# Kernel optimization log

Measured on AMD Instinct MI355X. Metric: run time of the kernel, lower is better.

## Reference

```python
import jax, jax.numpy as jnp
import numpy as np

B, T, C, H = 4, 2048, 1024, 16


def setup_inputs() -> dict:
    key = jax.random.key(0)
    ks = jax.random.split(key, 8)
    s = 0.02
    return {
        "xq": jax.random.normal(ks[0], (B, T, C), jnp.float32),
        "xk": jax.random.normal(ks[1], (B, T, C), jnp.float32),
        "xv": jax.random.normal(ks[2], (B, T, C), jnp.float32),
        "Wq": jax.random.normal(ks[3], (C, C), jnp.float32) * s,
        "Wk": jax.random.normal(ks[4], (C, C), jnp.float32) * s,
        "Wv": jax.random.normal(ks[5], (C, C), jnp.float32) * s,
        "Wo": jax.random.normal(ks[6], (C, C), jnp.float32) * s,
        "bo": jnp.zeros((C,), jnp.float32),
    }


def reference(xq, xk, xv, Wq, Wk, Wv, Wo, bo):
    # torch nn.Linear: y = x @ W.T
    q = xq @ Wq.T  # (B,T,C)
    k = xk @ Wk.T
    v = xv @ Wv.T
    hd = C // H
    # (B,T,C) -> (B,H,T,hd)
    q = q.reshape(B, T, H, hd).transpose(0, 2, 1, 3)
    k = k.reshape(B, T, H, hd).transpose(0, 2, 1, 3)
    v = v.reshape(B, T, H, hd).transpose(0, 2, 1, 3)
    scale = 1.0 / jnp.sqrt(jnp.asarray(hd, q.dtype))
    att = jnp.einsum("bhqd,bhkd->bhqk", q, k) * scale  # (B,H,T,T)
    causal = jnp.tril(jnp.ones((T, T), bool))
    att = jnp.where(causal, att, jnp.asarray(-jnp.inf, att.dtype))
    att = jax.nn.softmax(att, axis=-1)
    y = jnp.einsum("bhqk,bhkd->bhqd", att, v)  # (B,H,T,hd)
    y = y.transpose(0, 2, 1, 3).reshape(B, T, C)
    return y @ Wo.T + bo
```

## Files before the change

### kernel.cpp

```cpp
#include <hip/hip_runtime.h>
#include <stdint.h>

#define B_ 4
#define T_ 2048
#define C_ 1024
#define H_ 16
#define HD 64

typedef __attribute__((ext_vector_type(8))) short bf16x8;
typedef __attribute__((ext_vector_type(4))) short bf16x4;
typedef __attribute__((ext_vector_type(4))) float v4f;
typedef __attribute__((ext_vector_type(4))) uint32_t v4u;

static __device__ __forceinline__ short f2bf(float f) {
    union { float f; uint32_t u; } v; v.f = f;
    uint32_t u = v.u;
    uint32_t r = (u + 0x7fffu + ((u >> 16) & 1u)) >> 16;
    return (short)(r & 0xffffu);
}
static __device__ __forceinline__ uint32_t pack2(float x, float y) {
    uint32_t a = __float_as_uint(x) + 0x8000u;
    uint32_t b = __float_as_uint(y) + 0x8000u;
    return __builtin_amdgcn_perm(b, a, 0x07060302u);
}
static __device__ __forceinline__ uint32_t pack2t(float x, float y) {
    return __builtin_amdgcn_perm(__float_as_uint(y), __float_as_uint(x), 0x07060302u);
}
static __device__ __forceinline__ void gload_lds16(const void* g, void* l) {
    __builtin_amdgcn_global_load_lds(
        (const __attribute__((address_space(1))) void*)g,
        (__attribute__((address_space(3))) void*)l, 16, 0, 0);
}

__global__ __launch_bounds__(256) void convx(
    const float* __restrict__ x0, const float* __restrict__ x1,
    short* __restrict__ o0, short* __restrict__ o1,
    const float* __restrict__ w0, const float* __restrict__ w1,
    const float* __restrict__ w2, const float* __restrict__ w3,
    short* __restrict__ wout)
{
    int bid = blockIdx.x;
    const float* src; short* dst; size_t id;
    if (bid < 8192) {
        src = (bid < 4096) ? x0 : x1;
        dst = (bid < 4096) ? o0 : o1;
        id = (size_t)(bid & 4095) * 256 + threadIdx.x;
    } else {
        int wb = bid - 8192;
        int wi = wb >> 9;
        src = (wi == 0) ? w0 : (wi == 1) ? w1 : (wi == 2) ? w2 : w3;
        dst = wout + (size_t)wi * (C_ * C_);
        id = (size_t)(wb & 511) * 256 + threadIdx.x;
    }
    const float* p = src + id * 8;
    v4f a0 = *(const v4f*)p, a1 = *(const v4f*)(p + 4);
    v4u dv;
    dv[0] = pack2(a0[0], a0[1]); dv[1] = pack2(a0[2], a0[3]);
    dv[2] = pack2(a1[0], a1[1]); dv[3] = pack2(a1[2], a1[3]);
    *(v4u*)&dst[id * 8] = dv;
}


__global__ __launch_bounds__(256) void proj_gemm(
    const short* __restrict__ Xq, const short* __restrict__ Xk,
    const short* __restrict__ Wb, const float* __restrict__ xv,
    short* __restrict__ Qh, short* __restrict__ Kh, short* __restrict__ Vt,
    float qscale)
{
    const int K = 1024;
    __shared__ short As[128 * 64];
    __shared__ short Bs[128 * 64];
    const int t = threadIdx.x;
    const int w = t >> 6, l = t & 63, g = l >> 4, c = l & 15;
    const int wm = w & 1, wn = w >> 1;
    const int z = blockIdx.z;
    const int m0 = (z == 2 ? blockIdx.y : blockIdx.x) * 128;
    const int n0 = (z == 2 ? blockIdx.x : blockIdx.y) * 128;
    const short* Ab = (z == 0) ? Xq : (z == 1) ? Xk : (Wb + 2 * C_ * C_);
    const short* Bb = (z == 0) ? Wb : (Wb + C_ * C_);

    const int srow = l >> 3;
    const int sch = (l & 7) ^ (l >> 3);
    const int rch = c & 7;

    v4f acc[4][4];
#pragma unroll
    for (int i = 0; i < 4; ++i)
#pragma unroll
        for (int j = 0; j < 4; ++j) acc[i][j] = (v4f){0.f, 0.f, 0.f, 0.f};

    for (int k0 = 0; k0 < K; k0 += 64) {
        __syncthreads();
#pragma unroll
        for (int i = 0; i < 4; ++i) {
            int sp = w * 4 + i;
            gload_lds16(Ab + (size_t)(m0 + sp * 8 + srow) * K + k0 + sch * 8,
                        &As[sp * 512]);
        }
        if (z < 2) {
#pragma unroll
            for (int i = 0; i < 4; ++i) {
                int sp = w * 4 + i;
                gload_lds16(Bb + (size_t)(n0 + sp * 8 + srow) * K + k0 + sch * 8,
                            &Bs[sp * 512]);
            }
        } else {
#pragma unroll
            for (int i = 0; i < 4; ++i) {
                int id = i * 256 + t;
                int rr = id >> 3, cc = id & 7;
                const float* p = xv + (size_t)(n0 + rr) * K + k0 + cc * 8;
                v4f a0 = *(const v4f*)p, a1 = *(const v4f*)(p + 4);
                v4u dv;
                dv[0] = pack2(a0[0], a0[1]); dv[1] = pack2(a0[2], a0[3]);
                dv[2] = pack2(a1[0], a1[1]); dv[3] = pack2(a1[2], a1[3]);
                *(v4u*)&Bs[rr * 64 + ((cc ^ (rr & 7)) * 8)] = dv;
            }
        }
        __syncthreads();
#pragma unroll
        for (int s = 0; s < 2; ++s) {
            const int kch = ((4 * s + g) ^ rch) * 8;
            bf16x8 af[4], bfr[4];
#pragma unroll
            for (int i = 0; i < 4; ++i)
                af[i] = *(const bf16x8*)&As[(wm * 64 + i * 16 + c) * 64 + kch];
#pragma unroll
            for (int j = 0; j < 4; ++j)
                bfr[j] = *(const bf16x8*)&Bs[(wn * 64 + j * 16 + c) * 64 + kch];
#pragma unroll
            for (int i = 0; i < 4; ++i)
#pragma unroll
                for (int j = 0; j < 4; ++j)
                    acc[i][j] = __builtin_amdgcn_mfma_f32_16x16x32_bf16(af[i], bfr[j], acc[i][j], 0, 0, 0);
        }
    }
    if (z < 2) {
        short* Out = (z == 0) ? Qh : Kh;
        const float os = (z == 0) ? qscale : 1.0f;
#pragma unroll
        for (int i = 0; i < 4; ++i)
#pragma unroll
            for (int j = 0; j < 4; ++j)
#pragma unroll
                for (int r = 0; r < 4; ++r) {
                    int m = m0 + wm * 64 + i * 16 + g * 4 + r;
                    int n = n0 + wn * 64 + j * 16 + c;
                    int b = m >> 11, tt = m & (T_ - 1);
                    int h = n >> 6, d = n & 63;
                    Out[((size_t)(b * H_ + h) * T_ + tt) * HD + d] = f2bf(acc[i][j][r] * os);
                }
    } else {
#pragma unroll
        for (int i = 0; i < 4; ++i)
#pragma unroll
            for (int j = 0; j < 4; ++j)
#pragma unroll
                for (int r = 0; r < 4; ++r) {
                    int m = m0 + wm * 64 + i * 16 + g * 4 + r;
                    int n = n0 + wn * 64 + j * 16 + c;
                    int b = n >> 11, tt = n & (T_ - 1);
                    int h = m >> 6, d = m & 63;
                    Vt[((size_t)(b * H_ + h) * HD + d) * T_ + tt] = f2bf(acc[i][j][r]);
                }
    }
}

__global__ __launch_bounds__(256) void gemm_o(
    const short* __restrict__ Yb, const short* __restrict__ Wo,
    float* __restrict__ Out, const float* __restrict__ bias)
{
    const int K = 1024;
    __shared__ short As[128 * 64];
    __shared__ short Bs[128 * 64];
    const int t = threadIdx.x;
    const int w = t >> 6, l = t & 63, g = l >> 4, c = l & 15;
    const int wm = w & 1, wn = w >> 1;
    const int m0 = blockIdx.x * 128, n0 = blockIdx.y * 128;

    const int srow = l >> 3;
    const int sch = (l & 7) ^ (l >> 3);
    const int rch = c & 7;

    v4f acc[4][4];
#pragma unroll
    for (int i = 0; i < 4; ++i)
#pragma unroll
        for (int j = 0; j < 4; ++j) acc[i][j] = (v4f){0.f, 0.f, 0.f, 0.f};

    for (int k0 = 0; k0 < K; k0 += 64) {
        __syncthreads();
#pragma unroll
        for (int i = 0; i < 4; ++i) {
            int sp = w * 4 + i;
            gload_lds16(Yb + (size_t)(m0 + sp * 8 + srow) * K + k0 + sch * 8,
                        &As[sp * 512]);
            gload_lds16(Wo + (size_t)(n0 + sp * 8 + srow) * K + k0 + sch * 8,
                        &Bs[sp * 512]);
        }
        __syncthreads();
#pragma unroll
        for (int s = 0; s < 2; ++s) {
            const int kch = ((4 * s + g) ^ rch) * 8;
            bf16x8 af[4], bfr[4];
#pragma unroll
            for (int i = 0; i < 4; ++i)
                af[i] = *(const bf16x8*)&As[(wm * 64 + i * 16 + c) * 64 + kch];
#pragma unroll
            for (int j = 0; j < 4; ++j)
                bfr[j] = *(const bf16x8*)&Bs[(wn * 64 + j * 16 + c) * 64 + kch];
#pragma unroll
            for (int i = 0; i < 4; ++i)
#pragma unroll
                for (int j = 0; j < 4; ++j)
                    acc[i][j] = __builtin_amdgcn_mfma_f32_16x16x32_bf16(af[i], bfr[j], acc[i][j], 0, 0, 0);
        }
    }
#pragma unroll
    for (int i = 0; i < 4; ++i)
#pragma unroll
        for (int j = 0; j < 4; ++j)
#pragma unroll
            for (int r = 0; r < 4; ++r) {
                int m = m0 + wm * 64 + i * 16 + g * 4 + r;
                int n = n0 + wn * 64 + j * 16 + c;
                Out[(size_t)m * C_ + n] = acc[i][j][r] + bias[n];
            }
}

__global__ __launch_bounds__(256) void attn_kernel(
    const short* __restrict__ Q, const short* __restrict__ Kp,
    const short* __restrict__ Vt, short* __restrict__ Y)
{
    __shared__ short Ks[2 * 64 * 32];
    __shared__ short Vs[64 * 72];
    const int t = threadIdx.x;
    const int w = t >> 6, l = t & 63, g = l >> 4, c = l & 15;
    const int bid = blockIdx.x;
    const int slot = bid >> 3;
    const int p = slot & 15;
    const size_t bh = (size_t)((bid & 7) * 8 + (slot >> 4));

    const int srow = l >> 2;
    const int sch = (l & 3) ^ ((l >> 3) & 3);
    const int gs = (g ^ ((c >> 1) & 3)) * 8;

    bf16x8 ones;
#pragma unroll
    for (int i = 0; i < 8; ++i) ones[i] = (short)0x3F80;

    const int qtL = p, qtH = 31 - p;
    const int qbL = qtL * 64, qbH = qtH * 64;

    bf16x8 qL0, qL1, qH0, qH1;
    {
        const short* qp = &Q[(bh * T_ + qbL + w * 16 + c) * HD + g * 8];
        qL0 = *(const bf16x8*)qp;
        qL1 = *(const bf16x8*)(qp + 32);
    }
    {
        const short* qp = &Q[(bh * T_ + qbH + w * 16 + c) * HD + g * 8];
        qH0 = *(const bf16x8*)qp;
        qH1 = *(const bf16x8*)(qp + 32);
    }

    v4f OL[4], OH[4], accL, accH;
    accL = (v4f){0.f, 0.f, 0.f, 0.f};
    accH = (v4f){0.f, 0.f, 0.f, 0.f};
#pragma unroll
    for (int d = 0; d < 4; ++d) {
        OL[d] = (v4f){0.f, 0.f, 0.f, 0.f};
        OH[d] = (v4f){0.f, 0.f, 0.f, 0.f};
    }

    union pu { bf16x8 v; uint32_t u[4]; };

    for (int kb = 0; kb <= qtH; ++kb) {
        const int kbase = kb * 64;
        __syncthreads();
#pragma unroll
        for (int i = 0; i < 2; ++i) {
            int gi = w * 2 + i;
            int hk = gi >> 2, rb = gi & 3;
            const short* gp = &Kp[(bh * T_ + kbase + rb * 16 + srow) * HD + hk * 32 + sch * 8];
            gload_lds16(gp, &Ks[hk * 2048 + rb * 512]);
        }
#pragma unroll
        for (int i = 0; i < 2; ++i) {
            int id = i * 256 + t;
            int rr = id >> 3, cc = id & 7;
            *(bf16x8*)&Vs[rr * 72 + cc * 8] =
                *(const bf16x8*)&Vt[(bh * HD + rr) * T_ + kbase + cc * 8];
        }
        __syncthreads();

        const bool doL = (kb <= qtL);

        pu paH[2], paL[2];
        {
            float s2[4][4];
#pragma unroll
            for (int j = 0; j < 4; ++j) {
                bf16x8 kf0 = *(const bf16x8*)&Ks[(j * 16 + c) * 32 + gs];
                bf16x8 kf1 = *(const bf16x8*)&Ks[2048 + (j * 16 + c) * 32 + gs];
                v4f sa = (v4f){0.f, 0.f, 0.f, 0.f};
                sa = __builtin_amdgcn_mfma_f32_16x16x32_bf16(kf0, qH0, sa, 0, 0, 0);
                sa = __builtin_amdgcn_mfma_f32_16x16x32_bf16(kf1, qH1, sa, 0, 0, 0);
#pragma unroll
                for (int r = 0; r < 4; ++r) s2[j][r] = sa[r];
            }
            if (kb == qtH) {
                const int q = qbH + w * 16 + c;
#pragma unroll
                for (int j = 0; j < 4; ++j)
#pragma unroll
                    for (int r = 0; r < 4; ++r) {
                        int key = kbase + j * 16 + g * 4 + r;
                        if (key > q) s2[j][r] = -3.0e38f;
                    }
            }
#pragma unroll
            for (int s = 0; s < 2; ++s)
#pragma unroll
                for (int wi = 0; wi < 4; ++wi) {
                    int j = 2 * s + (wi >> 1);
                    int r0 = (wi & 1) * 2;
                    float x = __builtin_amdgcn_exp2f(s2[j][r0]);
                    float y = __builtin_amdgcn_exp2f(s2[j][r0 + 1]);
                    paH[s].u[wi] = pack2t(x, y);
                }
        }
        if (doL) {
            float s2[4][4];
#pragma unroll
            for (int j = 0; j < 4; ++j) {
                bf16x8 kf0 = *(const bf16x8*)&Ks[(j * 16 + c) * 32 + gs];
                bf16x8 kf1 = *(const bf16x8*)&Ks[2048 + (j * 16 + c) * 32 + gs];
                v4f sa = (v4f){0.f, 0.f, 0.f, 0.f};
                sa = __builtin_amdgcn_mfma_f32_16x16x32_bf16(kf0, qL0, sa, 0, 0, 0);
                sa = __builtin_amdgcn_mfma_f32_16x16x32_bf16(kf1, qL1, sa, 0, 0, 0);
#pragma unroll
                for (int r = 0; r < 4; ++r) s2[j][r] = sa[r];
            }
            if (kb == qtL) {
                const int q = qbL + w * 16 + c;
#pragma unroll
                for (int j = 0; j < 4; ++j)
#pragma unroll
                    for (int r = 0; r < 4; ++r) {
                        int key = kbase + j * 16 + g * 4 + r;
                        if (key > q) s2[j][r] = -3.0e38f;
                    }
            }
#pragma unroll
            for (int s = 0; s < 2; ++s)
#pragma unroll
                for (int wi = 0; wi < 4; ++wi) {
                    int j = 2 * s + (wi >> 1);
                    int r0 = (wi & 1) * 2;
                    float x = __builtin_amdgcn_exp2f(s2[j][r0]);
                    float y = __builtin_amdgcn_exp2f(s2[j][r0 + 1]);
                    paL[s].u[wi] = pack2t(x, y);
                }
#pragma unroll
            for (int s = 0; s < 2; ++s) {
#pragma unroll
                for (int d = 0; d < 4; ++d) {
                    const short* vp = &Vs[(d * 16 + c) * 72 + s * 32 + g * 4];
                    union { bf16x8 v8; bf16x4 v4[2]; } vu;
                    vu.v4[0] = *(const bf16x4*)vp;
                    vu.v4[1] = *(const bf16x4*)(vp + 16);
                    OH[d] = __builtin_amdgcn_mfma_f32_16x16x32_bf16(paH[s].v, vu.v8, OH[d], 0, 0, 0);
                    OL[d] = __builtin_amdgcn_mfma_f32_16x16x32_bf16(paL[s].v, vu.v8, OL[d], 0, 0, 0);
                }
                accH = __builtin_amdgcn_mfma_f32_16x16x32_bf16(paH[s].v, ones, accH, 0, 0, 0);
                accL = __builtin_amdgcn_mfma_f32_16x16x32_bf16(paL[s].v, ones, accL, 0, 0, 0);
            }
        } else {
#pragma unroll
            for (int s = 0; s < 2; ++s) {
#pragma unroll
                for (int d = 0; d < 4; ++d) {
                    const short* vp = &Vs[(d * 16 + c) * 72 + s * 32 + g * 4];
                    union { bf16x8 v8; bf16x4 v4[2]; } vu;
                    vu.v4[0] = *(const bf16x4*)vp;
                    vu.v4[1] = *(const bf16x4*)(vp + 16);
                    OH[d] = __builtin_amdgcn_mfma_f32_16x16x32_bf16(paH[s].v, vu.v8, OH[d], 0, 0, 0);
                }
                accH = __builtin_amdgcn_mfma_f32_16x16x32_bf16(paH[s].v, ones, accH, 0, 0, 0);
            }
        }
    }
#pragma unroll
    for (int r = 0; r < 4; ++r) {
        float rlL = 1.0f / accL[r];
        float rlH = 1.0f / accH[r];
        size_t baseoff = ((size_t)(bh >> 4) * T_ + w * 16 + g * 4 + r) * C_ + (bh & 15) * HD;
        size_t offL = baseoff + (size_t)qbL * C_;
        size_t offH = baseoff + (size_t)qbH * C_;
#pragma unroll
        for (int d = 0; d < 4; ++d) {
            Y[offL + d * 16 + c] = f2bf(OL[d][r] * rlL);
            Y[offH + d * 16 + c] = f2bf(OH[d][r] * rlH);
        }
    }
}

extern "C" void kernel_launch(void* const* d_in, const int* in_sizes, int n_in,
                              void* d_out, int out_size, void* d_ws, size_t ws_size,
                              hipStream_t stream) {
    const float* xq = (const float*)d_in[0];
    const float* xk = (const float*)d_in[1];
    const float* xv = (const float*)d_in[2];
    const float* Wq = (const float*)d_in[3];
    const float* Wk = (const float*)d_in[4];
    const float* Wv = (const float*)d_in[5];
    const float* Wo = (const float*)d_in[6];
    const float* bo = (const float*)d_in[7];

    const size_t NE = (size_t)B_ * H_ * T_ * HD;
    const size_t WE = (size_t)C_ * C_;
    short* Qh    = (short*)d_ws;
    short* Kh    = Qh + NE;
    short* slotA = Kh + NE;
    short* slotB = slotA + NE;
    short* Wbf   = slotB + NE;
    short* Vt    = (short*)d_out;

    const float qscale = 0.18033688011112042f;
    dim3 blk(256);

    hipLaunchKernelGGL(convx, dim3(10240), blk, 0, stream,
                       xq, xk, slotA, slotB, Wq, Wk, Wv, Wo, Wbf);
    hipLaunchKernelGGL(proj_gemm, dim3(64, 8, 3), blk, 0, stream,
                       slotA, slotB, Wbf, xv, Qh, Kh, Vt, qscale);
    hipLaunchKernelGGL(attn_kernel, dim3(B_ * H_ * (T_ / 128)), blk, 0, stream,
                       Qh, Kh, Vt, slotA);
    hipLaunchKernelGGL(gemm_o, dim3(64, 8), blk, 0, stream,
                       slotA, Wbf + 3 * WE, (float*)d_out, bo);
}
```

Measured before the change: 312.1 us.

## Double-buffer LDS tiles in projection and output GEMMs to overlap loads

Both GEMM kernels now keep two LDS buffers for the A and B tiles. The next k-slice is issued as direct-to-LDS global loads (or, for the V path, as register loads packed after compute) while MFMA runs on the current buffer, with one waitcnt plus barrier per half-step instead of two syncthreads per iteration. This is meant to hide global-load latency behind compute. In exchange, LDS use doubles to 64KB per block, which may lower occupancy, and the V path holds more prefetch registers.

```diff
diff --git a/kernel.cpp b/kernel.cpp
--- a/kernel.cpp
+++ b/kernel.cpp
@@ -68,8 +68,8 @@
     float qscale)
 {
     const int K = 1024;
-    __shared__ short As[128 * 64];
-    __shared__ short Bs[128 * 64];
+    __shared__ short As[2][128 * 64];
+    __shared__ short Bs[2][128 * 64];
     const int t = threadIdx.x;
     const int w = t >> 6, l = t & 63, g = l >> 4, c = l & 15;
     const int wm = w & 1, wn = w >> 1;
@@ -78,6 +78,8 @@
     const int n0 = (z == 2 ? blockIdx.x : blockIdx.y) * 128;
     const short* Ab = (z == 0) ? Xq : (z == 1) ? Xk : (Wb + 2 * C_ * C_);
     const short* Bb = (z == 0) ? Wb : (Wb + C_ * C_);
+    const short* Agb = Ab + (size_t)m0 * K;
+    const short* Bgb = Bb + (size_t)n0 * K;
 
     const int srow = l >> 3;
     const int sch = (l & 7) ^ (l >> 3);
@@ -89,52 +91,95 @@
 #pragma unroll
         for (int j = 0; j < 4; ++j) acc[i][j] = (v4f){0.f, 0.f, 0.f, 0.f};
 
-    for (int k0 = 0; k0 < K; k0 += 64) {
-        __syncthreads();
+    v4f pb0[4], pb1[4];
+
+    auto stage4 = [&](short* dst, const short* gbase, int kk) {
 #pragma unroll
         for (int i = 0; i < 4; ++i) {
             int sp = w * 4 + i;
-            gload_lds16(Ab + (size_t)(m0 + sp * 8 + srow) * K + k0 + sch * 8,
-                        &As[sp * 512]);
-        }
-        if (z < 2) {
-#pragma unroll
-            for (int i = 0; i < 4; ++i) {
-                int sp = w * 4 + i;
-                gload_lds16(Bb + (size_t)(n0 + sp * 8 + srow) * K + k0 + sch * 8,
-                            &Bs[sp * 512]);
-            }
-        } else {
-#pragma unroll
-            for (int i = 0; i < 4; ++i) {
-                int id = i * 256 + t;
-                int rr = id >> 3, cc = id & 7;
-                const float* p = xv + (size_t)(n0 + rr) * K + k0 + cc * 8;
-                v4f a0 = *(const v4f*)p, a1 = *(const v4f*)(p + 4);
-                v4u dv;
-                dv[0] = pack2(a0[0], a0[1]); dv[1] = pack2(a0[2], a0[3]);
-                dv[2] = pack2(a1[0], a1[1]); dv[3] = pack2(a1[2], a1[3]);
-                *(v4u*)&Bs[rr * 64 + ((cc ^ (rr & 7)) * 8)] = dv;
-            }
-        }
-        __syncthreads();
+            gload_lds16(gbase + (size_t)(sp * 8 + srow) * K + kk + sch * 8,
+                        dst + sp * 512);
+        }
+    };
+    auto loadB = [&](int kk) {
+#pragma unroll
+        for (int i = 0; i < 4; ++i) {
+            int id = i * 256 + t;
+            int rr = id >> 3, cc = id & 7;
+            const float* pp = xv + (size_t)(n0 + rr) * K + kk + cc * 8;
+            pb0[i] = *(const v4f*)pp;
+            pb1[i] = *(const v4f*)(pp + 4);
+        }
+    };
+    auto packB = [&](short* bsb) {
+#pragma unroll
+        for (int i = 0; i < 4; ++i) {
+            int id = i * 256 + t;
+            int rr = id >> 3, cc = id & 7;
+            v4u dv;
+            dv[0] = pack2(pb0[i][0], pb0[i][1]); dv[1] = pack2(pb0[i][2], pb0[i][3]);
+            dv[2] = pack2(pb1[i][0], pb1[i][1]); dv[3] = pack2(pb1[i][2], pb1[i][3]);
+            *(v4u*)&bsb[rr * 64 + ((cc ^ (rr & 7)) * 8)] = dv;
+        }
+    };
+    auto compute = [&](const short* asb, const short* bsb) {
 #pragma unroll
         for (int s = 0; s < 2; ++s) {
             const int kch = ((4 * s + g) ^ rch) * 8;
             bf16x8 af[4], bfr[4];
 #pragma unroll
             for (int i = 0; i < 4; ++i)
-                af[i] = *(const bf16x8*)&As[(wm * 64 + i * 16 + c) * 64 + kch];
+                af[i] = *(const bf16x8*)&asb[(wm * 64 + i * 16 + c) * 64 + kch];
 #pragma unroll
             for (int j = 0; j < 4; ++j)
-                bfr[j] = *(const bf16x8*)&Bs[(wn * 64 + j * 16 + c) * 64 + kch];
+                bfr[j] = *(const bf16x8*)&bsb[(wn * 64 + j * 16 + c) * 64 + kch];
 #pragma unroll
             for (int i = 0; i < 4; ++i)
 #pragma unroll
                 for (int j = 0; j < 4; ++j)
                     acc[i][j] = __builtin_amdgcn_mfma_f32_16x16x32_bf16(af[i], bfr[j], acc[i][j], 0, 0, 0);
         }
-    }
+    };
+
+    if (z < 2) {
+        stage4(&As[0][0], Agb, 0);
+        stage4(&Bs[0][0], Bgb, 0);
+    } else {
+        loadB(0);
+        stage4(&As[0][0], Agb, 0);
+        packB(&Bs[0][0]);
+    }
+    asm volatile("s_waitcnt vmcnt(0) lgkmcnt(0)" ::: "memory");
+    __builtin_amdgcn_s_barrier();
+
+    for (int k0 = 0; k0 < K; k0 += 128) {
+        if (z < 2) {
+            stage4(&As[1][0], Agb, k0 + 64);
+            stage4(&Bs[1][0], Bgb, k0 + 64);
+        } else {
+            loadB(k0 + 64);
+            stage4(&As[1][0], Agb, k0 + 64);
+        }
+        compute(&As[0][0], &Bs[0][0]);
+        if (z == 2) packB(&Bs[1][0]);
+        asm volatile("s_waitcnt vmcnt(0) lgkmcnt(0)" ::: "memory");
+        __builtin_amdgcn_s_barrier();
+        const bool pre = (k0 + 128 < K);
+        if (pre) {
+            if (z < 2) {
+                stage4(&As[0][0], Agb, k0 + 128);
+                stage4(&Bs[0][0], Bgb, k0 + 128);
+            } else {
+                loadB(k0 + 128);
+                stage4(&As[0][0], Agb, k0 + 128);
+            }
+        }
+        compute(&As[1][0], &Bs[1][0]);
+        if (pre && z == 2) packB(&Bs[0][0]);
+        asm volatile("s_waitcnt vmcnt(0) lgkmcnt(0)" ::: "memory");
+        __builtin_amdgcn_s_barrier();
+    }
+
     if (z < 2) {
         short* Out = (z == 0) ? Qh : Kh;
         const float os = (z == 0) ? qscale : 1.0f;
@@ -171,12 +216,14 @@
     float* __restrict__ Out, const float* __restrict__ bias)
 {
     const int K = 1024;
-    __shared__ short As[128 * 64];
-    __shared__ short Bs[128 * 64];
+    __shared__ short As[2][128 * 64];
+    __shared__ short Bs[2][128 * 64];
     const int t = threadIdx.x;
     const int w = t >> 6, l = t & 63, g = l >> 4, c = l & 15;
     const int wm = w & 1, wn = w >> 1;
     const int m0 = blockIdx.x * 128, n0 = blockIdx.y * 128;
+    const short* Agb = Yb + (size_t)m0 * K;
+    const short* Bgb = Wo + (size_t)n0 * K;
 
     const int srow = l >> 3;
     const int sch = (l & 7) ^ (l >> 3);
@@ -188,34 +235,54 @@
 #pragma unroll
         for (int j = 0; j < 4; ++j) acc[i][j] = (v4f){0.f, 0.f, 0.f, 0.f};
 
-    for (int k0 = 0; k0 < K; k0 += 64) {
-        __syncthreads();
+    auto stage4 = [&](short* dst, const short* gbase, int kk) {
 #pragma unroll
         for (int i = 0; i < 4; ++i) {
             int sp = w * 4 + i;
-            gload_lds16(Yb + (size_t)(m0 + sp * 8 + srow) * K + k0 + sch * 8,
-                        &As[sp * 512]);
-            gload_lds16(Wo + (size_t)(n0 + sp * 8 + srow) * K + k0 + sch * 8,
-                        &Bs[sp * 512]);
-        }
-        __syncthreads();
+            gload_lds16(gbase + (size_t)(sp * 8 + srow) * K + kk + sch * 8,
+                        dst + sp * 512);
+        }
+    };
+    auto compute = [&](const short* asb, const short* bsb) {
 #pragma unroll
         for (int s = 0; s < 2; ++s) {
             const int kch = ((4 * s + g) ^ rch) * 8;
             bf16x8 af[4], bfr[4];
 #pragma unroll
             for (int i = 0; i < 4; ++i)
-                af[i] = *(const bf16x8*)&As[(wm * 64 + i * 16 + c) * 64 + kch];
+                af[i] = *(const bf16x8*)&asb[(wm * 64 + i * 16 + c) * 64 + kch];
 #pragma unroll
             for (int j = 0; j < 4; ++j)
-                bfr[j] = *(const bf16x8*)&Bs[(wn * 64 + j * 16 + c) * 64 + kch];
+                bfr[j] = *(const bf16x8*)&bsb[(wn * 64 + j * 16 + c) * 64 + kch];
 #pragma unroll
             for (int i = 0; i < 4; ++i)
 #pragma unroll
                 for (int j = 0; j < 4; ++j)
                     acc[i][j] = __builtin_amdgcn_mfma_f32_16x16x32_bf16(af[i], bfr[j], acc[i][j], 0, 0, 0);
         }
-    }
+    };
+
+    stage4(&As[0][0], Agb, 0);
+    stage4(&Bs[0][0], Bgb, 0);
+    asm volatile("s_waitcnt vmcnt(0) lgkmcnt(0)" ::: "memory");
+    __builtin_amdgcn_s_barrier();
+
+    for (int k0 = 0; k0 < K; k0 += 128) {
+        stage4(&As[1][0], Agb, k0 + 64);
+        stage4(&Bs[1][0], Bgb, k0 + 64);
+        compute(&As[0][0], &Bs[0][0]);
+        asm volatile("s_waitcnt vmcnt(0) lgkmcnt(0)" ::: "memory");
+        __builtin_amdgcn_s_barrier();
+        const bool pre = (k0 + 128 < K);
+        if (pre) {
+            stage4(&As[0][0], Agb, k0 + 128);
+            stage4(&Bs[0][0], Bgb, k0 + 128);
+        }
+        compute(&As[1][0], &Bs[1][0]);
+        asm volatile("s_waitcnt vmcnt(0) lgkmcnt(0)" ::: "memory");
+        __builtin_amdgcn_s_barrier();
+    }
+
 #pragma unroll
     for (int i = 0; i < 4; ++i)
 #pragma unroll
```

Result: slower. 319.7 us (+2.5%).
